# Kernel optimization log

Hardware: AMD Instinct MI355X
Metric: run time of the kernel (lower is better)

The kernel has to match this reference:

```python
import jax, jax.numpy as jnp
import numpy as np

B, S, H = 4, 2048, 576
NH, NKV, HD = 9, 3, 64
GROUPS = NH // NKV
ROPE_THETA = 100000.0
MAX_POS = 8192


def _rope_tables():
    inv_freq = 1.0 / (ROPE_THETA ** (jnp.arange(0, HD, 2, dtype=jnp.float32) / HD))
    t = jnp.arange(MAX_POS, dtype=jnp.float32)
    freqs = jnp.outer(t, inv_freq)              # [MAX_POS, HD//2]
    emb = jnp.concatenate([freqs, freqs], axis=-1)  # [MAX_POS, HD]
    return jnp.cos(emb), jnp.sin(emb)


def _rotate_half(x):
    x1, x2 = x[..., : HD // 2], x[..., HD // 2 :]
    return jnp.concatenate([-x2, x1], axis=-1)


def setup_inputs() -> dict:
    key = jax.random.key(0)
    k1, k2, k3, k4, k5 = jax.random.split(key, 5)
    hidden_states = jax.random.normal(k1, (B, S, H), dtype=jnp.float32)
    # causal additive mask [B,1,S,S]: 0 where allowed, large negative above diagonal
    causal = jnp.triu(jnp.ones((S, S), dtype=bool), k=1)
    attention_mask = jnp.where(causal, jnp.float32(-1e9), jnp.float32(0.0))[None, None]
    attention_mask = jnp.broadcast_to(attention_mask, (B, 1, S, S))
    position_ids = jnp.broadcast_to(jnp.arange(S, dtype=jnp.int32)[None, :], (B, S))
    scale = 1.0 / np.sqrt(H)
    Wq = jax.random.normal(k2, (NH * HD, H), dtype=jnp.float32) * scale
    Wk = jax.random.normal(k3, (NKV * HD, H), dtype=jnp.float32) * scale
    Wv = jax.random.normal(k4, (NKV * HD, H), dtype=jnp.float32) * scale
    Wo = jax.random.normal(k5, (H, NH * HD), dtype=jnp.float32) * scale
    return {"hidden_states": hidden_states, "attention_mask": attention_mask,
            "position_ids": position_ids, "Wq": Wq, "Wk": Wk, "Wv": Wv, "Wo": Wo}


def reference(hidden_states, attention_mask, position_ids, Wq, Wk, Wv, Wo):
    bsz, q_len, _ = hidden_states.shape
    cos_cached, sin_cached = _rope_tables()
    # projections (nn.Linear: x @ W.T), reshape to [B, heads, S, HD]
    q = (hidden_states @ Wq.T).reshape(bsz, q_len, NH, HD).transpose(0, 2, 1, 3)
    k = (hidden_states @ Wk.T).reshape(bsz, q_len, NKV, HD).transpose(0, 2, 1, 3)
    v = (hidden_states @ Wv.T).reshape(bsz, q_len, NKV, HD).transpose(0, 2, 1, 3)
    # RoPE: gather cos/sin per position, broadcast over heads
    cos = cos_cached[position_ids][:, None]  # [B,1,S,HD]
    sin = sin_cached[position_ids][:, None]
    q = q * cos + _rotate_half(q) * sin
    k = k * cos + _rotate_half(k) * sin
    # GQA: repeat_interleave kv heads
    k = jnp.repeat(k, GROUPS, axis=1)  # [B,NH,S,HD]
    v = jnp.repeat(v, GROUPS, axis=1)
    scores = jnp.einsum('bhqd,bhkd->bhqk', q, k) / np.sqrt(HD)
    scores = scores + attention_mask
    probs = jax.nn.softmax(scores.astype(jnp.float32), axis=-1).astype(q.dtype)
    attn = jnp.einsum('bhqk,bhkd->bhqd', probs, v)
    attn = attn.transpose(0, 2, 1, 3).reshape(bsz, q_len, NH * HD)
    return attn @ Wo.T
```

## Files before the change

### kernel.cpp

```cpp
#include <hip/hip_runtime.h>
#include <hip/hip_bf16.h>
#include <math.h>

#define Bsz 4
#define Slen 2048
#define Hdim 576
#define NH 9
#define NKV 3
#define HD 64

typedef __bf16 bf16_t;
typedef __bf16 bf16x8 __attribute__((ext_vector_type(8)));
typedef float f32x4 __attribute__((ext_vector_type(4)));
typedef float f32x16 __attribute__((ext_vector_type(16)));
typedef unsigned int u32;
typedef unsigned int u32x4 __attribute__((ext_vector_type(4)));

static __device__ __forceinline__ bf16x8 load_cvt8(const float* __restrict__ src){
  float4 f0 = *reinterpret_cast<const float4*>(src);
  float4 f1 = *reinterpret_cast<const float4*>(src + 4);
  bf16x8 v;
  v[0]=(bf16_t)f0.x; v[1]=(bf16_t)f0.y; v[2]=(bf16_t)f0.z; v[3]=(bf16_t)f0.w;
  v[4]=(bf16_t)f1.x; v[5]=(bf16_t)f1.y; v[6]=(bf16_t)f1.z; v[7]=(bf16_t)f1.w;
  return v;
}

static __device__ __forceinline__ void gload16(const bf16_t* g, bf16_t* l){
  __builtin_amdgcn_global_load_lds((const __attribute__((address_space(1))) void*)g,
                                   (__attribute__((address_space(3))) void*)l, 16, 0, 0);
}

static __device__ __forceinline__ float xhalf_sum(float x){
  return x + __shfl_xor(x, 32, 64);
}

__global__ void setup_kernel(const float* __restrict__ X,
                             const float* __restrict__ Wq,
                             const float* __restrict__ Wk,
                             const float* __restrict__ Wv,
                             const float* __restrict__ Wo,
                             bf16_t* __restrict__ Xb,
                             bf16_t* __restrict__ Wb,
                             bf16_t* __restrict__ Wob,
                             float* __restrict__ cost,
                             float* __restrict__ sint)
{
  const int bid = blockIdx.x;
  if (bid < 256){
    int i = bid * 256 + threadIdx.x;
    int j = i & 31;
    int p = i >> 5;
    double invf = pow(100000.0, -(double)j / 32.0);
    double ang = (double)p * invf;
    cost[i] = (float)cos(ang);
    sint[i] = (float)sin(ang);
    return;
  }
  const int NX  = 8192 * 576 / 8;
  const int NWq = 576 * 576 / 8;
  const int NWk = 192 * 576 / 8;
  int i = (bid - 256) * 256 + threadIdx.x;
  const int total = NX + NWq + 2 * NWk + NWq;
  if (i >= total) return;
  const float* src; bf16_t* dst; int off;
  if (i < NX)                    { src = X;  dst = Xb;            off = i; }
  else if (i < NX + NWq)         { src = Wq; dst = Wb;            off = i - NX; }
  else if (i < NX + NWq + NWk)   { src = Wk; dst = Wb + 331776;   off = i - NX - NWq; }
  else if (i < NX + NWq + 2*NWk) { src = Wv; dst = Wb + 442368;   off = i - NX - NWq - NWk; }
  else                           { src = Wo; dst = Wob;           off = i - NX - NWq - 2*NWk; }
  *reinterpret_cast<bf16x8*>(dst + (size_t)off * 8) = load_cvt8(src + (size_t)off * 8);
}

__launch_bounds__(256)
__global__ void qkv_gemm_kernel(const bf16_t* __restrict__ Xb,
                                const bf16_t* __restrict__ Wb,
                                const int* __restrict__ pos_ids,
                                const float* __restrict__ cost,
                                const float* __restrict__ sint,
                                float qscale,
                                bf16_t* __restrict__ qbuf,
                                bf16_t* __restrict__ kbuf,
                                bf16_t* __restrict__ vtbuf)
{
  __shared__ bf16_t Ald[2][128 * 64];
  __shared__ bf16_t Bld[2][64 * 64];
  const int t = threadIdx.x, l = t & 63, w = t >> 6;
  const int wm = w >> 1, wn = w & 1;
  const int lane16 = l & 15, grp = l >> 4;
  const int m0 = blockIdx.x * 128;
  const int nt = blockIdx.y;
  const int nrow0 = nt * 64;

  const int sr = l >> 3;
  const int sc = ((l & 7) ^ sr) * 8;

  f32x4 acc[4][2];
  #pragma unroll
  for (int mi = 0; mi < 4; ++mi)
    #pragma unroll
    for (int ni = 0; ni < 2; ++ni)
      acc[mi][ni] = (f32x4){0.f, 0.f, 0.f, 0.f};

  auto STAGE = [&](int kt, int buf){
    const int k0 = kt * 64;
    #pragma unroll
    for (int u = 0; u < 4; ++u)
      gload16(Xb + (size_t)(m0 + w * 32 + u * 8 + sr) * Hdim + k0 + sc,
              &Ald[buf][(w * 32 + u * 8) * 64]);
    #pragma unroll
    for (int u = 0; u < 2; ++u)
      gload16(Wb + (size_t)(nrow0 + w * 16 + u * 8 + sr) * Hdim + k0 + sc,
              &Bld[buf][(w * 16 + u * 8) * 64]);
  };

  STAGE(0, 0);
  asm volatile("s_waitcnt vmcnt(0)" ::: "memory");
  __syncthreads();

  const int sl7 = lane16 & 7;
  for (int kt = 0; kt < 9; ++kt){
    const int buf = kt & 1;
    if (kt + 1 < 9) STAGE(kt + 1, buf ^ 1);
    #pragma unroll
    for (int ks = 0; ks < 2; ++ks){
      bf16x8 a[4], bb[2];
      #pragma unroll
      for (int mi = 0; mi < 4; ++mi){
        int row = wm * 64 + mi * 16 + lane16;
        a[mi] = *reinterpret_cast<const bf16x8*>(&Ald[buf][row * 64 + (((ks * 4 + grp) ^ sl7) * 8)]);
      }
      #pragma unroll
      for (int ni = 0; ni < 2; ++ni){
        int row = ni * 32 + wn * 16 + lane16;
        bb[ni] = *reinterpret_cast<const bf16x8*>(&Bld[buf][row * 64 + (((ks * 4 + grp) ^ sl7) * 8)]);
      }
      #pragma unroll
      for (int mi = 0; mi < 4; ++mi)
        #pragma unroll
        for (int ni = 0; ni < 2; ++ni)
          acc[mi][ni] = __builtin_amdgcn_mfma_f32_16x16x32_bf16(a[mi], bb[ni], acc[mi][ni], 0, 0, 0);
    }
    if (kt + 1 < 9){
      asm volatile("s_waitcnt vmcnt(0)" ::: "memory");
      __syncthreads();
    }
  }

  const int d = wn * 16 + lane16;
  #pragma unroll
  for (int mi = 0; mi < 4; ++mi){
    #pragma unroll
    for (int j = 0; j < 4; ++j){
      int m = m0 + wm * 64 + mi * 16 + grp * 4 + j;
      int b = m >> 11;
      int s = m & 2047;
      float x0 = acc[mi][0][j], x1 = acc[mi][1][j];
      if (nt < 12){
        int pos = pos_ids[b * Slen + s];
        float c = cost[pos * 32 + d], sn = sint[pos * 32 + d];
        float scale = (nt < 9) ? qscale : 1.0f;
        float o0 = (x0 * c - x1 * sn) * scale;
        float o1 = (x1 * c + x0 * sn) * scale;
        x0 = o0; x1 = o1;
      }
      if (nt < 9){
        bf16_t* dst = qbuf + (((size_t)b * NH + nt) * Slen + s) * HD;
        dst[d] = (bf16_t)x0; dst[d + 32] = (bf16_t)x1;
      } else if (nt < 12){
        bf16_t* dst = kbuf + (((size_t)b * NKV + (nt - 9)) * Slen + s) * HD;
        dst[d] = (bf16_t)x0; dst[d + 32] = (bf16_t)x1;
      } else {
        bf16_t* dst = vtbuf + ((size_t)b * NKV + (nt - 12)) * HD * Slen + s;
        dst[(size_t)d * Slen] = (bf16_t)x0; dst[(size_t)(d + 32) * Slen] = (bf16_t)x1;
      }
    }
  }
}

__launch_bounds__(128)
__global__ void flash_attn_kernel(const bf16_t* __restrict__ qbuf,
                                  const bf16_t* __restrict__ kbuf,
                                  const bf16_t* __restrict__ vtbuf,
                                  u32* __restrict__ part_O,
                                  float* __restrict__ part_ml)
{
  __shared__ bf16_t Kld[2][32 * 64];
  __shared__ bf16_t Vld[2][64 * 32];
  const int t = threadIdx.x, l = t & 63, w = t >> 6;
  const int l32 = l & 31, hi = l >> 5;

  const int flat = blockIdx.x;
  const int v = flat / 36;
  const int bh = flat % 36;
  const int qt = 31 - (v >> 1);
  const int seg = v & 1;
  const int t0 = seg * (qt + 1);
  const int t1 = t0 + qt + 1;
  const int b = bh / NH, h = bh % NH, kvh = h / (NH / NKV);

  const bf16_t* qp = qbuf + ((size_t)b * NH + h) * Slen * HD;
  const bf16_t* kp = kbuf + ((size_t)b * NKV + kvh) * Slen * HD;
  const bf16_t* vp = vtbuf + ((size_t)b * NKV + kvh) * HD * Slen;

  const int krow = l >> 3;
  const int ksc  = ((l & 7) ^ krow) * 8;
  const int vrow = l >> 2;
  const int vsc  = ((l & 3) ^ ((vrow >> 1) & 3)) * 8;

  auto STAGE = [&](int kt, int buf){
    const int k0 = kt * 32;
    #pragma unroll
    for (int u = 0; u < 2; ++u){
      int ub = w * 2 + u;
      gload16(kp + (size_t)(k0 + ub * 8 + krow) * HD + ksc, &Kld[buf][ub * 512]);
    }
    #pragma unroll
    for (int u = 0; u < 2; ++u){
      int ub = w * 2 + u;
      gload16(vp + (size_t)(ub * 16 + vrow) * Slen + k0 + vsc, &Vld[buf][ub * 512]);
    }
  };

  const int q0 = qt * 64 + w * 32;
  bf16x8 aq[4];
  #pragma unroll
  for (int ds = 0; ds < 4; ++ds)
    aq[ds] = *reinterpret_cast<const bf16x8*>(qp + (size_t)(q0 + l32) * HD + ds * 16 + hi * 8);

  STAGE(t0, 0);
  if (t0 + 1 < t1) STAGE(t0 + 1, 1);

  f32x16 acco[2];
  #pragma unroll
  for (int db = 0; db < 2; ++db)
    #pragma unroll
    for (int r = 0; r < 16; ++r) acco[db][r] = 0.f;
  float lhalf = 0.f;

  const int dt = 2 * qt + w;
  for (int kb = t0; kb < t1; ++kb){
    const int cur = (kb - t0) & 1;
    const bool rem1 = (kb + 1 < t1), rem2 = (kb + 2 < t1);

    if (rem1) asm volatile("s_waitcnt vmcnt(6)" ::: "memory");
    else      asm volatile("s_waitcnt vmcnt(2)" ::: "memory");
    __syncthreads();

    u32x4 pa0, pa1;
    if (kb <= dt){
      f32x16 sacc;
      #pragma unroll
      for (int r = 0; r < 16; ++r) sacc[r] = 0.f;
      __builtin_amdgcn_s_setprio(1);
      #pragma unroll
      for (int ds = 0; ds < 4; ++ds){
        bf16x8 ak = *reinterpret_cast<const bf16x8*>(
            &Kld[cur][l32 * 64 + (((ds * 2 + hi) ^ (l32 & 7)) * 8)]);
        sacc = __builtin_amdgcn_mfma_f32_32x32x16_bf16(ak, aq[ds], sacc, 0, 0, 0);
      }
      __builtin_amdgcn_s_setprio(0);

      if (kb == dt){
        #pragma unroll
        for (int r = 0; r < 16; ++r){
          int crow = (r & 3) + 8 * (r >> 2) + 4 * hi;
          if (crow > l32) sacc[r] = -1e30f;
        }
      }

      #pragma unroll
      for (int r = 0; r < 16; ++r)
        sacc[r] = __builtin_amdgcn_exp2f(sacc[r]);
      float s0 = sacc[0] + sacc[1],  s1 = sacc[2] + sacc[3];
      float s2 = sacc[4] + sacc[5],  s3 = sacc[6] + sacc[7];
      float s4 = sacc[8] + sacc[9],  s5 = sacc[10] + sacc[11];
      float s6 = sacc[12] + sacc[13], s7 = sacc[14] + sacc[15];
      s0 += s1; s2 += s3; s4 += s5; s6 += s7;
      lhalf += (s0 + s2) + (s4 + s6);

      u32 wv[8];
      #pragma unroll
      for (int j = 0; j < 8; ++j){
        float lo = sacc[2 * j], hp = sacc[2 * j + 1];
        asm("v_cvt_pk_bf16_f32 %0, %1, %2" : "=v"(wv[j]) : "v"(lo), "v"(hp));
      }
      asm volatile("v_permlane32_swap_b32 %0, %1" : "+v"(wv[0]), "+v"(wv[2]));
      asm volatile("v_permlane32_swap_b32 %0, %1" : "+v"(wv[1]), "+v"(wv[3]));
      asm volatile("v_permlane32_swap_b32 %0, %1" : "+v"(wv[4]), "+v"(wv[6]));
      asm volatile("v_permlane32_swap_b32 %0, %1" : "+v"(wv[5]), "+v"(wv[7]));
      pa0 = (u32x4){wv[0], wv[1], wv[2], wv[3]};
      pa1 = (u32x4){wv[4], wv[5], wv[6], wv[7]};
    }

    if (rem1) asm volatile("s_waitcnt vmcnt(4)" ::: "memory");
    else      asm volatile("s_waitcnt vmcnt(0)" ::: "memory");
    __syncthreads();

    if (kb <= dt){
      __builtin_amdgcn_s_setprio(1);
      #pragma unroll
      for (int ks = 0; ks < 2; ++ks){
        #pragma unroll
        for (int db = 0; db < 2; ++db){
          bf16x8 av = *reinterpret_cast<const bf16x8*>(
              &Vld[cur][(db * 32 + l32) * 32 + (((ks * 2 + hi) ^ ((l32 >> 1) & 3)) * 8)]);
          acco[db] = __builtin_amdgcn_mfma_f32_32x32x16_bf16(
              av, __builtin_bit_cast(bf16x8, ks ? pa1 : pa0), acco[db], 0, 0, 0);
        }
      }
      __builtin_amdgcn_s_setprio(0);
    }

    if (rem2){
      __syncthreads();
      STAGE(kb + 2, cur);
    }
  }

  const float lrun = xhalf_sum(lhalf);

  const int slot = (bh * 32 + qt) * 2 + seg;
  u32* po = part_O + ((size_t)slot * 2 + w) * 1024;
  float* pml = part_ml + ((size_t)slot * 2 + w) * 64;
  #pragma unroll
  for (int db = 0; db < 2; ++db){
    #pragma unroll
    for (int j = 0; j < 8; ++j){
      int r = 2 * j;
      int d = db * 32 + (r & 3) + 8 * (r >> 2) + 4 * hi;
      u32 pw;
      float lo = acco[db][r], hp = acco[db][r + 1];
      asm("v_cvt_pk_bf16_f32 %0, %1, %2" : "=v"(pw) : "v"(lo), "v"(hp));
      po[(d >> 1) * 32 + l32] = pw;
    }
  }
  if (hi == 0){ pml[l32] = 0.f; pml[32 + l32] = lrun; }
}

__launch_bounds__(128)
__global__ void combine_kernel(const u32* __restrict__ part_O,
                               const float* __restrict__ part_ml,
                               bf16_t* __restrict__ attn_out)
{
  const int idx = blockIdx.x;
  const int bh = idx % 36, qt = idx / 36;
  const int b = bh / NH, h = bh % NH;
  const int t = threadIdx.x;
  const int q = t & 31, wg = (t >> 5) & 1, half = t >> 6;
  const int slot0 = (bh * 32 + qt) * 2;

  const float* pml0 = part_ml + ((size_t)(slot0 + 0) * 2 + wg) * 64;
  const float* pml1 = part_ml + ((size_t)(slot0 + 1) * 2 + wg) * 64;
  float m1 = pml0[q], l1 = pml0[32 + q];
  float m2 = pml1[q], l2 = pml1[32 + q];
  float m = fmaxf(m1, m2);
  float a1 = __builtin_amdgcn_exp2f(m1 - m);
  float a2 = __builtin_amdgcn_exp2f(m2 - m);
  float linv = 1.0f / (l1 * a1 + l2 * a2);
  a1 *= linv; a2 *= linv;

  const u32* po0 = part_O + ((size_t)(slot0 + 0) * 2 + wg) * 1024;
  const u32* po1 = part_O + ((size_t)(slot0 + 1) * 2 + wg) * 1024;
  const int s = qt * 64 + wg * 32 + q;
  bf16_t* orow = attn_out + ((size_t)b * Slen + s) * (NH * HD) + h * HD;

  #pragma unroll
  for (int u = 0; u < 16; ++u){
    int dp = half * 16 + u;
    u32 v1 = po0[dp * 32 + q], v2 = po1[dp * 32 + q];
    float lo = a1 * __builtin_bit_cast(float, v1 << 16)
             + a2 * __builtin_bit_cast(float, v2 << 16);
    float hv = a1 * __builtin_bit_cast(float, v1 & 0xffff0000u)
             + a2 * __builtin_bit_cast(float, v2 & 0xffff0000u);
    u32 pw;
    asm("v_cvt_pk_bf16_f32 %0, %1, %2" : "=v"(pw) : "v"(lo), "v"(hv));
    *reinterpret_cast<u32*>(orow + 2 * dp) = pw;
  }
}

__launch_bounds__(256)
__global__ void out_gemm_kernel(const bf16_t* __restrict__ A,
                                const bf16_t* __restrict__ Wob,
                                float* __restrict__ out)
{
  __shared__ bf16_t Ald[2][128 * 64];
  __shared__ bf16_t Bld[2][64 * 64];
  const int t = threadIdx.x, l = t & 63, w = t >> 6;
  const int wm = w >> 1, wn = w & 1;
  const int lane16 = l & 15, grp = l >> 4;
  const int m0 = blockIdx.x * 128;
  const int nt = blockIdx.y;
  const int nrow0 = nt * 64;

  const int sr = l >> 3;
  const int sc = ((l & 7) ^ sr) * 8;

  f32x4 acc[4][2];
  #pragma unroll
  for (int mi = 0; mi < 4; ++mi)
    #pragma unroll
    for (int ni = 0; ni < 2; ++ni)
      acc[mi][ni] = (f32x4){0.f, 0.f, 0.f, 0.f};

  auto STAGE = [&](int kt, int buf){
    const int k0 = kt * 64;
    #pragma unroll
    for (int u = 0; u < 4; ++u)
      gload16(A + (size_t)(m0 + w * 32 + u * 8 + sr) * Hdim + k0 + sc,
              &Ald[buf][(w * 32 + u * 8) * 64]);
    #pragma unroll
    for (int u = 0; u < 2; ++u)
      gload16(Wob + (size_t)(nrow0 + w * 16 + u * 8 + sr) * Hdim + k0 + sc,
              &Bld[buf][(w * 16 + u * 8) * 64]);
  };

  STAGE(0, 0);
  asm volatile("s_waitcnt vmcnt(0)" ::: "memory");
  __syncthreads();

  const int sl7 = lane16 & 7;
  for (int kt = 0; kt < 9; ++kt){
    const int buf = kt & 1;
    if (kt + 1 < 9) STAGE(kt + 1, buf ^ 1);
    #pragma unroll
    for (int ks = 0; ks < 2; ++ks){
      bf16x8 a[4], bb[2];
      #pragma unroll
      for (int mi = 0; mi < 4; ++mi){
        int row = wm * 64 + mi * 16 + lane16;
        a[mi] = *reinterpret_cast<const bf16x8*>(&Ald[buf][row * 64 + (((ks * 4 + grp) ^ sl7) * 8)]);
      }
      #pragma unroll
      for (int ni = 0; ni < 2; ++ni){
        int row = wn * 32 + ni * 16 + lane16;
        bb[ni] = *reinterpret_cast<const bf16x8*>(&Bld[buf][row * 64 + (((ks * 4 + grp) ^ sl7) * 8)]);
      }
      #pragma unroll
      for (int mi = 0; mi < 4; ++mi)
        #pragma unroll
        for (int ni = 0; ni < 2; ++ni)
          acc[mi][ni] = __builtin_amdgcn_mfma_f32_16x16x32_bf16(a[mi], bb[ni], acc[mi][ni], 0, 0, 0);
    }
    if (kt + 1 < 9){
      asm volatile("s_waitcnt vmcnt(0)" ::: "memory");
      __syncthreads();
    }
  }

  #pragma unroll
  for (int mi = 0; mi < 4; ++mi){
    #pragma unroll
    for (int ni = 0; ni < 2; ++ni){
      #pragma unroll
      for (int j = 0; j < 4; ++j){
        int m = m0 + wm * 64 + mi * 16 + grp * 4 + j;
        int n = nrow0 + wn * 32 + ni * 16 + lane16;
        out[(size_t)m * Hdim + n] = acc[mi][ni][j];
      }
    }
  }
}

extern "C" void kernel_launch(void* const* d_in, const int* in_sizes, int n_in,
                              void* d_out, int out_size, void* d_ws, size_t ws_size,
                              hipStream_t stream) {
  const float* X   = (const float*)d_in[0];
  const int* pos   = (const int*)d_in[2];
  const float* Wq  = (const float*)d_in[3];
  const float* Wk  = (const float*)d_in[4];
  const float* Wv  = (const float*)d_in[5];
  const float* Wo  = (const float*)d_in[6];
  float* out = (float*)d_out;

  char* ws = (char*)d_ws;
  float* cost = (float*)ws;
  float* sint = (float*)(ws + 262144);
  bf16_t* qb  = (bf16_t*)(ws + 524288);
  bf16_t* kb  = qb + (size_t)Bsz * NH * Slen * HD;
  bf16_t* vt  = kb + (size_t)Bsz * NKV * Slen * HD;
  bf16_t* Xb  = vt + (size_t)Bsz * NKV * Slen * HD;
  bf16_t* ab  = Xb;
  bf16_t* Wb  = Xb + (size_t)8192 * 576;
  bf16_t* Wob = Wb + (size_t)960 * 576;
  u32*  part_O  = (u32*)(Wob + (size_t)576 * 576);
  float* part_ml = (float*)(part_O + (size_t)2304 * 2 * 1024);

  const float QSCALE = 0.125f * 1.44269504088896f;

  setup_kernel<<<dim3(256 + 2736), dim3(256), 0, stream>>>(X, Wq, Wk, Wv, Wo, Xb, Wb, Wob, cost, sint);
  qkv_gemm_kernel<<<dim3(64, 15), dim3(256), 0, stream>>>(Xb, Wb, pos, cost, sint, QSCALE, qb, kb, vt);
  flash_attn_kernel<<<dim3(2304), dim3(128), 0, stream>>>(qb, kb, vt, part_O, part_ml);
  combine_kernel<<<dim3(1152), dim3(128), 0, stream>>>(part_O, part_ml, ab);
  out_gemm_kernel<<<dim3(64, 9), dim3(256), 0, stream>>>(ab, Wob, out);
}
```

Before: 110.1 us.

## Fuse split-KV combine into output projection GEMM A-tile staging

Removes the separate combine kernel and its intermediate bf16 attention buffer. The output GEMM now reads the two partial attention results per row and sums them. It normalises by the summed row denominators, relying on the stored running max being zero. It then writes the bf16 A tile into shared memory itself. This saves one launch and one write-plus-read of the intermediate, but each of the 9 N-tile blocks re-reads and re-combines the partials through narrow, strided 32-bit global loads held in registers. The global loads can also no longer go straight into shared memory.

```diff
diff --git a/kernel.cpp b/kernel.cpp
--- a/kernel.cpp
+++ b/kernel.cpp
@@ -337,49 +337,9 @@
   if (hi == 0){ pml[l32] = 0.f; pml[32 + l32] = lrun; }
 }
 
-__launch_bounds__(128)
-__global__ void combine_kernel(const u32* __restrict__ part_O,
-                               const float* __restrict__ part_ml,
-                               bf16_t* __restrict__ attn_out)
-{
-  const int idx = blockIdx.x;
-  const int bh = idx % 36, qt = idx / 36;
-  const int b = bh / NH, h = bh % NH;
-  const int t = threadIdx.x;
-  const int q = t & 31, wg = (t >> 5) & 1, half = t >> 6;
-  const int slot0 = (bh * 32 + qt) * 2;
-
-  const float* pml0 = part_ml + ((size_t)(slot0 + 0) * 2 + wg) * 64;
-  const float* pml1 = part_ml + ((size_t)(slot0 + 1) * 2 + wg) * 64;
-  float m1 = pml0[q], l1 = pml0[32 + q];
-  float m2 = pml1[q], l2 = pml1[32 + q];
-  float m = fmaxf(m1, m2);
-  float a1 = __builtin_amdgcn_exp2f(m1 - m);
-  float a2 = __builtin_amdgcn_exp2f(m2 - m);
-  float linv = 1.0f / (l1 * a1 + l2 * a2);
-  a1 *= linv; a2 *= linv;
-
-  const u32* po0 = part_O + ((size_t)(slot0 + 0) * 2 + wg) * 1024;
-  const u32* po1 = part_O + ((size_t)(slot0 + 1) * 2 + wg) * 1024;
-  const int s = qt * 64 + wg * 32 + q;
-  bf16_t* orow = attn_out + ((size_t)b * Slen + s) * (NH * HD) + h * HD;
-
-  #pragma unroll
-  for (int u = 0; u < 16; ++u){
-    int dp = half * 16 + u;
-    u32 v1 = po0[dp * 32 + q], v2 = po1[dp * 32 + q];
-    float lo = a1 * __builtin_bit_cast(float, v1 << 16)
-             + a2 * __builtin_bit_cast(float, v2 << 16);
-    float hv = a1 * __builtin_bit_cast(float, v1 & 0xffff0000u)
-             + a2 * __builtin_bit_cast(float, v2 & 0xffff0000u);
-    u32 pw;
-    asm("v_cvt_pk_bf16_f32 %0, %1, %2" : "=v"(pw) : "v"(lo), "v"(hv));
-    *reinterpret_cast<u32*>(orow + 2 * dp) = pw;
-  }
-}
-
 __launch_bounds__(256)
-__global__ void out_gemm_kernel(const bf16_t* __restrict__ A,
+__global__ void out_gemm_kernel(const u32* __restrict__ part_O,
+                                const float* __restrict__ part_ml,
                                 const bf16_t* __restrict__ Wob,
                                 float* __restrict__ out)
 {
@@ -394,34 +354,101 @@
 
   const int sr = l >> 3;
   const int sc = ((l & 7) ^ sr) * 8;
-
-  f32x4 acc[4][2];
-  #pragma unroll
-  for (int mi = 0; mi < 4; ++mi)
-    #pragma unroll
-    for (int ni = 0; ni < 2; ++ni)
-      acc[mi][ni] = (f32x4){0.f, 0.f, 0.f, 0.f};
-
-  auto STAGE = [&](int kt, int buf){
+  const int dp0 = sc >> 1;
+
+  int rowq[4]; size_t poff0[4], poff1[4]; float lpt[4];
+  u32 a1v[4][4], a2v[4][4];
+
+  auto AROWS = [&](int kt){
+    #pragma unroll
+    for (int u = 0; u < 4; ++u){
+      int m = m0 + w * 32 + u * 8 + sr;
+      int b = m >> 11, s2 = m & 2047;
+      int qt = s2 >> 6, wg = (s2 >> 5) & 1, q = s2 & 31;
+      int slot0 = ((b * NH + kt) * 32 + qt) * 2;
+      poff0[u] = ((size_t)(slot0 + 0) * 2 + wg) * 1024 + q;
+      poff1[u] = ((size_t)(slot0 + 1) * 2 + wg) * 1024 + q;
+      rowq[u] = q;
+    }
+  };
+
+  auto AISSUE = [&](int kt){
+    AROWS(kt);
+    #pragma unroll
+    for (int u = 0; u < 4; ++u){
+      #pragma unroll
+      for (int i = 0; i < 4; ++i){
+        a1v[u][i] = part_O[poff0[u] + (size_t)(dp0 + i) * 32];
+        a2v[u][i] = part_O[poff1[u] + (size_t)(dp0 + i) * 32];
+      }
+      float l1 = part_ml[(poff0[u] - rowq[u]) / 16 + 32 + rowq[u]];
+      (void)l1;
+    }
+  };
+  (void)AISSUE;
+
+  auto ASTAGE_ISSUE = [&](int kt){
+    AROWS(kt);
+    #pragma unroll
+    for (int u = 0; u < 4; ++u){
+      #pragma unroll
+      for (int i = 0; i < 4; ++i){
+        a1v[u][i] = part_O[poff0[u] + (size_t)(dp0 + i) * 32];
+        a2v[u][i] = part_O[poff1[u] + (size_t)(dp0 + i) * 32];
+      }
+      size_t ml0 = (poff0[u] - rowq[u]) / 1024 * 64;
+      size_t ml1 = (poff1[u] - rowq[u]) / 1024 * 64;
+      lpt[u] = part_ml[ml0 + 32 + rowq[u]] + part_ml[ml1 + 32 + rowq[u]];
+    }
+  };
+
+  auto ADSWRITE = [&](int buf){
+    #pragma unroll
+    for (int u = 0; u < 4; ++u){
+      float linv = 1.0f / lpt[u];
+      bf16_t o8[8];
+      #pragma unroll
+      for (int i = 0; i < 4; ++i){
+        float lo = __builtin_bit_cast(float, a1v[u][i] << 16)
+                 + __builtin_bit_cast(float, a2v[u][i] << 16);
+        float hp = __builtin_bit_cast(float, a1v[u][i] & 0xffff0000u)
+                 + __builtin_bit_cast(float, a2v[u][i] & 0xffff0000u);
+        o8[2 * i]     = (bf16_t)(lo * linv);
+        o8[2 * i + 1] = (bf16_t)(hp * linv);
+      }
+      *reinterpret_cast<bf16x8*>(&Ald[buf][(w * 32 + u * 8 + sr) * 64 + (l & 7) * 8]) =
+          *reinterpret_cast<bf16x8*>(o8);
+    }
+  };
+
+  auto BSTAGE = [&](int kt, int buf){
     const int k0 = kt * 64;
-    #pragma unroll
-    for (int u = 0; u < 4; ++u)
-      gload16(A + (size_t)(m0 + w * 32 + u * 8 + sr) * Hdim + k0 + sc,
-              &Ald[buf][(w * 32 + u * 8) * 64]);
     #pragma unroll
     for (int u = 0; u < 2; ++u)
       gload16(Wob + (size_t)(nrow0 + w * 16 + u * 8 + sr) * Hdim + k0 + sc,
               &Bld[buf][(w * 16 + u * 8) * 64]);
   };
 
-  STAGE(0, 0);
+  f32x4 acc[4][2];
+  #pragma unroll
+  for (int mi = 0; mi < 4; ++mi)
+    #pragma unroll
+    for (int ni = 0; ni < 2; ++ni)
+      acc[mi][ni] = (f32x4){0.f, 0.f, 0.f, 0.f};
+
+  ASTAGE_ISSUE(0);
+  BSTAGE(0, 0);
   asm volatile("s_waitcnt vmcnt(0)" ::: "memory");
+  ADSWRITE(0);
   __syncthreads();
 
   const int sl7 = lane16 & 7;
   for (int kt = 0; kt < 9; ++kt){
     const int buf = kt & 1;
-    if (kt + 1 < 9) STAGE(kt + 1, buf ^ 1);
+    if (kt + 1 < 9){
+      ASTAGE_ISSUE(kt + 1);
+      BSTAGE(kt + 1, buf ^ 1);
+    }
     #pragma unroll
     for (int ks = 0; ks < 2; ++ks){
       bf16x8 a[4], bb[2];
@@ -443,6 +470,7 @@
     }
     if (kt + 1 < 9){
       asm volatile("s_waitcnt vmcnt(0)" ::: "memory");
+      ADSWRITE(buf ^ 1);
       __syncthreads();
     }
   }
@@ -479,7 +507,6 @@
   bf16_t* kb  = qb + (size_t)Bsz * NH * Slen * HD;
   bf16_t* vt  = kb + (size_t)Bsz * NKV * Slen * HD;
   bf16_t* Xb  = vt + (size_t)Bsz * NKV * Slen * HD;
-  bf16_t* ab  = Xb;
   bf16_t* Wb  = Xb + (size_t)8192 * 576;
   bf16_t* Wob = Wb + (size_t)960 * 576;
   u32*  part_O  = (u32*)(Wob + (size_t)576 * 576);
@@ -490,6 +517,5 @@
   setup_kernel<<<dim3(256 + 2736), dim3(256), 0, stream>>>(X, Wq, Wk, Wv, Wo, Xb, Wb, Wob, cost, sint);
   qkv_gemm_kernel<<<dim3(64, 15), dim3(256), 0, stream>>>(Xb, Wb, pos, cost, sint, QSCALE, qb, kb, vt);
   flash_attn_kernel<<<dim3(2304), dim3(128), 0, stream>>>(qb, kb, vt, part_O, part_ml);
-  combine_kernel<<<dim3(1152), dim3(128), 0, stream>>>(part_O, part_ml, ab);
-  out_gemm_kernel<<<dim3(64, 9), dim3(256), 0, stream>>>(ab, Wob, out);
-}
+  out_gemm_kernel<<<dim3(64, 9), dim3(256), 0, stream>>>(part_O, part_ml, Wob, out);
+}
```

Measured after the change: 185.6 us. +68.5%, slower.
